# Performance work log

Hardware: AMD Instinct MI355X
Metric: run time of the kernel (lower is better)

The kernel has to match this reference:

```python
import jax, jax.numpy as jnp
import numpy as np

N = 100000   # nodes
E = 640000   # edges
F = 128      # num_features
D = 128      # dim
G = 128      # graphs in batch
BN_EPS = 1e-5


def setup_inputs() -> dict:
    key = jax.random.key(0)
    ks = jax.random.split(key, 16)
    lin = lambda k, i, o: (jax.random.normal(k, (i, o), jnp.float32) / np.sqrt(i)).astype(jnp.float32)
    inp = {
        "x": jax.random.normal(ks[0], (N, F), jnp.float32),
        "edge_index": jax.random.randint(ks[1], (2, E), 0, N),
        "batch": jnp.sort(jax.random.randint(ks[2], (N,), 0, G)),
        # layer 0: Linear(F,D)-ReLU-Linear(D,D), BN(D)
        "W0a": lin(ks[3], F, D), "b0a": jnp.zeros((D,), jnp.float32),
        "W0b": lin(ks[4], D, D), "b0b": jnp.zeros((D,), jnp.float32),
        "g0": jnp.ones((D,), jnp.float32), "be0": jnp.zeros((D,), jnp.float32),
        # layer 1: Linear(D,D)-ReLU-Linear(D,D), BN(D)
        "W1a": lin(ks[5], D, D), "b1a": jnp.zeros((D,), jnp.float32),
        "W1b": lin(ks[6], D, D), "b1b": jnp.zeros((D,), jnp.float32),
        "g1": jnp.ones((D,), jnp.float32), "be1": jnp.zeros((D,), jnp.float32),
        # layer 2: Linear(D,D)-ReLU-Linear(D,1), BN(1)
        "W2a": lin(ks[7], D, D), "b2a": jnp.zeros((D,), jnp.float32),
        "W2b": lin(ks[8], D, 1), "b2b": jnp.zeros((1,), jnp.float32),
        "g2": jnp.ones((1,), jnp.float32), "be2": jnp.zeros((1,), jnp.float32),
    }
    return inp


def _gin_layer(x, src, dst, Wa, ba, Wb, bb, g, be, relu_out):
    # GINConv (eps=0): h = x + sum_{j in N(i)} x_j, then MLP, then BN (train-mode stats)
    agg = jax.ops.segment_sum(x[src], dst, num_segments=N)
    h = x + agg
    h = jax.nn.relu(h @ Wa + ba) @ Wb + bb
    mu = jnp.mean(h, axis=0)
    var = jnp.mean((h - mu) ** 2, axis=0)  # biased var (torch BN normalization)
    h = (h - mu) * jax.lax.rsqrt(var + BN_EPS) * g + be
    return jax.nn.relu(h) if relu_out else h


def reference(x, edge_index, batch,
              W0a, b0a, W0b, b0b, g0, be0,
              W1a, b1a, W1b, b1b, g1, be1,
              W2a, b2a, W2b, b2b, g2, be2):
    src, dst = edge_index[0], edge_index[1]
    h = _gin_layer(x, src, dst, W0a, b0a, W0b, b0b, g0, be0, True)
    h = _gin_layer(h, src, dst, W1a, b1a, W1b, b1b, g1, be1, True)
    h = _gin_layer(h, src, dst, W2a, b2a, W2b, b2b, g2, be2, False)  # [N,1], no final ReLU
    # segment softmax over graphs, temperature 5.0 (PyG softmax semantics)
    z = h / 5.0
    m = jax.ops.segment_max(z, batch, num_segments=G)
    ez = jnp.exp(z - m[batch])
    s = jax.ops.segment_sum(ez, batch, num_segments=G)
    return ez / (s[batch] + 1e-16)
```

## Files before the change

### kernel.cpp

```cpp
#include <hip/hip_runtime.h>
#include <math.h>

#define NN 100000
#define EE 640000
#define GG 128
#define BN_EPS 1e-5f
#define NBLK 98

typedef __attribute__((ext_vector_type(8))) short short8;
typedef __attribute__((ext_vector_type(4))) float f32x4;


__device__ __forceinline__ short f2bf(float f) {
    unsigned u = __float_as_uint(f);
    u += 0x7fffu + ((u >> 16) & 1);
    return (short)(u >> 16);
}
__device__ __forceinline__ float bf2f(short s) {
    return __uint_as_float(((unsigned)(unsigned short)s) << 16);
}
__device__ __forceinline__ int swz(int row, int chunk) {
    return row * 128 + ((chunk ^ (row & 15)) << 3);
}
__device__ __forceinline__ int swze(int row, int col) {
    return row * 128 + (((col >> 3) ^ (row & 15)) << 3) + (col & 7);
}

__global__ void k_setup(const float* __restrict__ x,
                        const float* __restrict__ W0a, const float* __restrict__ W0b,
                        const float* __restrict__ W1a, const float* __restrict__ W1b,
                        const float* __restrict__ W2a, short* __restrict__ Wt,
                        short* __restrict__ Xbf, int* __restrict__ deg,
                        float* __restrict__ smf) {
    int idx = blockIdx.x * 256 + threadIdx.x;
    if (idx < 81920) {
        int wi = idx >> 14, r = idx & 16383;
        const float* W = (wi == 0) ? W0a : (wi == 1) ? W0b : (wi == 2) ? W1a
                        : (wi == 3) ? W1b : W2a;
        int k = r >> 7, n = r & 127;
        int ch = n >> 6, ct = (n >> 4) & 3, r16 = n & 15;
        int kc = k >> 3, kk = kc >> 2, q = kc & 3, e = k & 7;
        int lane = r16 + (q << 4);
        Wt[wi * 16384 + ((((ch * 4 + ct) * 4 + kk) * 64 + lane) << 3) + e] =
            f2bf(W[k * 128 + n]);
    }
    if (idx < NN) deg[idx] = 0;
    if (idx < 4112) smf[idx] = 0.0f;
    if (idx < 1600000) {
        const float4* xr = (const float4*)x + (size_t)idx * 2;
        float4 v0 = xr[0], v1 = xr[1];
        short8 o;
        o[0] = f2bf(v0.x); o[1] = f2bf(v0.y); o[2] = f2bf(v0.z); o[3] = f2bf(v0.w);
        o[4] = f2bf(v1.x); o[5] = f2bf(v1.y); o[6] = f2bf(v1.z); o[7] = f2bf(v1.w);
        *(short8*)(Xbf + (size_t)idx * 8) = o;
    }
}

__global__ void k_hist(const int* __restrict__ ei, int* __restrict__ deg) {
    int e = blockIdx.x * 256 + threadIdx.x;
    if (e < EE) atomicAdd(&deg[ei[EE + e]], 1);
}

__global__ __launch_bounds__(1024) void k_scan1(const int* __restrict__ deg,
                                                int* __restrict__ offs,
                                                int* __restrict__ bsums) {
    __shared__ int sm[1024];
    int t = threadIdx.x;
    int i = blockIdx.x * 1024 + t;
    int v = (i < NN) ? deg[i] : 0;
    sm[t] = v;
    __syncthreads();
    for (int off = 1; off < 1024; off <<= 1) {
        int add = (t >= off) ? sm[t - off] : 0;
        __syncthreads();
        sm[t] += add;
        __syncthreads();
    }
    if (i < NN) offs[i] = sm[t] - v;
    if (t == 1023) bsums[blockIdx.x] = sm[1023];
}

__global__ __launch_bounds__(1024) void k_scan3(int* __restrict__ offs,
                                                const int* __restrict__ bsums,
                                                int* __restrict__ pos) {
    __shared__ int smb[128];
    __shared__ int baseS;
    int t = threadIdx.x;
    if (t < 128) smb[t] = (t < NBLK) ? bsums[t] : 0;
    __syncthreads();
    if (t == 0) {
        int b = 0;
        for (int i = 0; i < (int)blockIdx.x; ++i) b += smb[i];
        baseS = b;
    }
    __syncthreads();
    int i = blockIdx.x * 1024 + t;
    if (i < NN) {
        int o = offs[i] + baseS;
        offs[i] = o;
        pos[i] = o;
    }
    if (i == 0) offs[NN] = EE;
}

__global__ void k_fill(const int* __restrict__ ei, int* __restrict__ pos,
                       int* __restrict__ csr) {
    int e = blockIdx.x * 256 + threadIdx.x;
    if (e < EE) {
        int d = ei[EE + e];
        int p = atomicAdd(&pos[d], 1);
        csr[p] = ei[e];
    }
}

template <int MODE>
__global__ __launch_bounds__(256, 4) void k_gmlp(const short* __restrict__ hin,
                                                 const int* __restrict__ offs,
                                                 const int* __restrict__ csr,
                                                 const float* __restrict__ rep,
                                                 const float* __restrict__ g,
                                                 const float* __restrict__ be,
                                                 const short* __restrict__ Wta,
                                                 const float* __restrict__ ba,
                                                 const short* __restrict__ Wtb,
                                                 const float* __restrict__ bb,
                                                 short* __restrict__ hout,
                                                 float* __restrict__ statsRep,
                                                 const float* __restrict__ w2,
                                                 const float* __restrict__ b2,
                                                 float* __restrict__ z,
                                                 float* __restrict__ s2rep) {
    __shared__ short Asb[8192];
    __shared__ float parS[128], parH[128];
    __shared__ float redS[1024];
    const int t = threadIdx.x;
    const int row0 = blockIdx.x * 64;
    const int lane = t & 63, wave = t >> 6;
    const int r16 = lane & 15, q = lane >> 4;
    const int rh = wave & 1, ch = wave >> 1;
    const int RA = rh * 32, CB = ch * 64;
    const int l = t & 15;

    if constexpr (MODE != 0) {
        if (t < 128) {
            float s = 0.f, ss = 0.f;
#pragma unroll
            for (int r = 0; r < 8; ++r) {
                s += rep[r * 256 + t];
                ss += rep[r * 256 + 128 + t];
            }
            const float inv = 1.0f / (float)NN;
            float mu = s * inv;
            float var = ss * inv - mu * mu;
            float sc = g[t] / sqrtf(var + BN_EPS);
            parS[t] = sc;
            parH[t] = be[t] - mu * sc;
        }
        __syncthreads();
    }

    const short* wA = Wta + (size_t)((ch * 1024 + lane) << 3);
    const short* wB = (MODE != 2) ? (Wtb + (size_t)((ch * 1024 + lane) << 3)) : nullptr;

    float sc8[8], sh8[8];
    if constexpr (MODE != 0) {
#pragma unroll
        for (int j = 0; j < 8; ++j) { sc8[j] = parS[l * 8 + j]; sh8[j] = parH[l * 8 + j]; }
    }
#pragma unroll
    for (int p = 0; p < 4; ++p) {
        int r = p * 16 + (t >> 4);
        int gr = row0 + r;
        float f8[8] = {0.f, 0.f, 0.f, 0.f, 0.f, 0.f, 0.f, 0.f};
        if (gr < NN) {
            int j0 = offs[gr], j1 = offs[gr + 1];
            short8 v = *(const short8*)(hin + (size_t)gr * 128 + l * 8);
#pragma unroll
            for (int k = 0; k < 8; ++k)
                f8[k] = (MODE != 0) ? fmaxf(fmaf(bf2f(v[k]), sc8[k], sh8[k]), 0.f) : bf2f(v[k]);
            int jlast = j1 - 1;
            for (int j = j0; j < j1; j += 8) {
                int ii[8];
                float mk[8];
                ii[0] = j;
                mk[0] = 1.f;
#pragma unroll
                for (int u = 1; u < 8; ++u) {
                    ii[u] = min(j + u, jlast);
                    mk[u] = (j + u <= jlast) ? 1.f : 0.f;
                }
                int sidx[8];
#pragma unroll
                for (int u = 0; u < 8; ++u) sidx[u] = csr[ii[u]];
                short8 w[8];
#pragma unroll
                for (int u = 0; u < 8; ++u)
                    w[u] = *(const short8*)(hin + (size_t)sidx[u] * 128 + l * 8);
#pragma unroll
                for (int k = 0; k < 8; ++k) {
                    if constexpr (MODE != 0) {
                        f8[k] += fmaxf(fmaf(bf2f(w[0][k]), sc8[k], sh8[k]), 0.f);
#pragma unroll
                        for (int u = 1; u < 8; ++u)
                            f8[k] = fmaf(mk[u], fmaxf(fmaf(bf2f(w[u][k]), sc8[k], sh8[k]), 0.f), f8[k]);
                    } else {
                        f8[k] += bf2f(w[0][k]);
#pragma unroll
                        for (int u = 1; u < 8; ++u)
                            f8[k] = fmaf(mk[u], bf2f(w[u][k]), f8[k]);
                    }
                }
            }
        }
        short8 o;
#pragma unroll
        for (int k = 0; k < 8; ++k) o[k] = f2bf(f8[k]);
        *(short8*)&Asb[swz(r, l)] = o;
    }
    __syncthreads();

    f32x4 acc[2][4];
#pragma unroll
    for (int rt = 0; rt < 2; ++rt)
#pragma unroll
        for (int ct = 0; ct < 4; ++ct) acc[rt][ct] = (f32x4)0.f;
#pragma unroll
    for (int kk = 0; kk < 4; ++kk) {
        short8 b[4], a[2];
#pragma unroll
        for (int ct = 0; ct < 4; ++ct)
            b[ct] = *(const short8*)(wA + ((ct * 4 + kk) << 9));
#pragma unroll
        for (int rt = 0; rt < 2; ++rt)
            a[rt] = *(const short8*)&Asb[swz(RA + rt * 16 + r16, kk * 4 + q)];
#pragma unroll
        for (int rt = 0; rt < 2; ++rt)
#pragma unroll
            for (int ct = 0; ct < 4; ++ct)
                acc[rt][ct] = __builtin_amdgcn_mfma_f32_16x16x32_bf16(a[rt], b[ct], acc[rt][ct], 0, 0, 0);
    }
    __syncthreads();

    float bav[4];
#pragma unroll
    for (int ct = 0; ct < 4; ++ct) bav[ct] = ba[CB + ct * 16 + r16];
#pragma unroll
    for (int rt = 0; rt < 2; ++rt)
#pragma unroll
        for (int ct = 0; ct < 4; ++ct)
#pragma unroll
            for (int rg = 0; rg < 4; ++rg) {
                float m = fmaxf(acc[rt][ct][rg] + bav[ct], 0.f);
                Asb[swze(RA + rt * 16 + q * 4 + rg, CB + ct * 16 + r16)] = f2bf(m);
            }
    __syncthreads();

    if constexpr (MODE == 2) {
        const int rr = t >> 4;
        float4 w0 = ((const float4*)w2)[l * 2];
        float4 w1 = ((const float4*)w2)[l * 2 + 1];
        float b2v = b2[0];
        float s = 0.f, ss = 0.f;
#pragma unroll
        for (int p = 0; p < 4; ++p) {
            int r = p * 16 + rr;
            int gr = row0 + r;
            short8 v = *(const short8*)&Asb[swz(r, l)];
            float pp = bf2f(v[0]) * w0.x + bf2f(v[1]) * w0.y + bf2f(v[2]) * w0.z +
                       bf2f(v[3]) * w0.w + bf2f(v[4]) * w1.x + bf2f(v[5]) * w1.y +
                       bf2f(v[6]) * w1.z + bf2f(v[7]) * w1.w;
#pragma unroll
            for (int off = 1; off < 16; off <<= 1) pp += __shfl_xor(pp, off, 16);
            if (l == 0 && gr < NN) {
                float h2 = pp + b2v;
                z[gr] = h2;
                s += h2;
                ss += h2 * h2;
            }
        }
        s += __shfl_xor(s, 16); s += __shfl_xor(s, 32);
        ss += __shfl_xor(ss, 16); ss += __shfl_xor(ss, 32);
        if ((t & 63) == 0) { redS[wave * 2] = s; redS[wave * 2 + 1] = ss; }
        __syncthreads();
        if (t == 0) {
            float S = 0.f, SS = 0.f;
#pragma unroll
            for (int w = 0; w < 4; ++w) { S += redS[w * 2]; SS += redS[w * 2 + 1]; }
            int rp = (blockIdx.x & 7) * 2;
            unsafeAtomicAdd(&s2rep[rp], S);
            unsafeAtomicAdd(&s2rep[rp + 1], SS);
        }
        return;
    } else {
#pragma unroll
        for (int rt = 0; rt < 2; ++rt)
#pragma unroll
            for (int ct = 0; ct < 4; ++ct) acc[rt][ct] = (f32x4)0.f;
#pragma unroll
        for (int kk = 0; kk < 4; ++kk) {
            short8 b[4], a[2];
#pragma unroll
            for (int ct = 0; ct < 4; ++ct)
                b[ct] = *(const short8*)(wB + ((ct * 4 + kk) << 9));
#pragma unroll
            for (int rt = 0; rt < 2; ++rt)
                a[rt] = *(const short8*)&Asb[swz(RA + rt * 16 + r16, kk * 4 + q)];
#pragma unroll
            for (int rt = 0; rt < 2; ++rt)
#pragma unroll
                for (int ct = 0; ct < 4; ++ct)
                    acc[rt][ct] = __builtin_amdgcn_mfma_f32_16x16x32_bf16(a[rt], b[ct], acc[rt][ct], 0, 0, 0);
        }
        __syncthreads();

        float bbv[4];
#pragma unroll
        for (int ct = 0; ct < 4; ++ct) bbv[ct] = bb[CB + ct * 16 + r16];
        float s[4] = {0.f, 0.f, 0.f, 0.f}, ss[4] = {0.f, 0.f, 0.f, 0.f};
#pragma unroll
        for (int rt = 0; rt < 2; ++rt)
#pragma unroll
            for (int ct = 0; ct < 4; ++ct)
#pragma unroll
                for (int rg = 0; rg < 4; ++rg) {
                    int lr = RA + rt * 16 + q * 4 + rg;
                    int gr = row0 + lr;
                    float hv = acc[rt][ct][rg] + bbv[ct];
                    if (gr < NN) { s[ct] += hv; ss[ct] += hv * hv; }
                    Asb[swze(lr, CB + ct * 16 + r16)] = f2bf(hv);
                }
#pragma unroll
        for (int ct = 0; ct < 4; ++ct) {
            s[ct] += __shfl_xor(s[ct], 16);
            s[ct] += __shfl_xor(s[ct], 32);
            ss[ct] += __shfl_xor(ss[ct], 16);
            ss[ct] += __shfl_xor(ss[ct], 32);
        }
        if (lane < 16) {
#pragma unroll
            for (int ct = 0; ct < 4; ++ct) {
                int col = CB + ct * 16 + r16;
                redS[rh * 512 + col] = s[ct];
                redS[rh * 512 + 128 + col] = ss[ct];
            }
        }
        __syncthreads();
        if (t < 256) {
            float v = redS[t] + redS[512 + t];
            unsafeAtomicAdd(&statsRep[(blockIdx.x & 7) * 256 + t], v);
        }
#pragma unroll
        for (int i = 0; i < 4; ++i) {
            int f = i * 256 + t;
            int r = f >> 4, c8 = f & 15;
            int gr = row0 + r;
            if (gr < NN)
                *(short8*)(hout + (size_t)gr * 128 + c8 * 8) = *(const short8*)&Asb[swz(r, c8)];
        }
    }
}

__device__ __forceinline__ int lbound(const int* __restrict__ b, int val) {
    int lo = 0, hi = NN;
    while (lo < hi) {
        int m = (lo + hi) >> 1;
        if (b[m] < val) lo = m + 1; else hi = m;
    }
    return lo;
}

__global__ void k_softmax(const float* __restrict__ zr, const float* __restrict__ s2rep,
                          const float* __restrict__ g2, const float* __restrict__ be2,
                          const int* __restrict__ batch, float* __restrict__ out) {
    __shared__ float rb[4];
    const int g = blockIdx.x, t = threadIdx.x;
    const int lo = lbound(batch, g), hi = lbound(batch, g + 1);
    float s = 0.f, ssq = 0.f;
#pragma unroll
    for (int i = 0; i < 8; ++i) { s += s2rep[i * 2]; ssq += s2rep[i * 2 + 1]; }
    const float mu = s / (float)NN;
    const float var = ssq / (float)NN - mu * mu;
    const float sc = g2[0] / sqrtf(var + BN_EPS) * 0.2f;
    const float sh = (be2[0] - mu * g2[0] / sqrtf(var + BN_EPS)) * 0.2f;

    float m = -INFINITY;
    for (int i = lo + t; i < hi; i += 256) m = fmaxf(m, fmaf(zr[i], sc, sh));
#pragma unroll
    for (int off = 1; off < 64; off <<= 1) m = fmaxf(m, __shfl_xor(m, off, 64));
    if ((t & 63) == 0) rb[t >> 6] = m;
    __syncthreads();
    float gmax = fmaxf(fmaxf(rb[0], rb[1]), fmaxf(rb[2], rb[3]));
    __syncthreads();

    float sum = 0.f;
    for (int i = lo + t; i < hi; i += 256) {
        float e = expf(fmaf(zr[i], sc, sh) - gmax);
        out[i] = e;
        sum += e;
    }
#pragma unroll
    for (int off = 1; off < 64; off <<= 1) sum += __shfl_xor(sum, off, 64);
    if ((t & 63) == 0) rb[t >> 6] = sum;
    __syncthreads();
    float S = rb[0] + rb[1] + rb[2] + rb[3];
    float inv = 1.0f / (S + 1e-16f);
    for (int i = lo + t; i < hi; i += 256) out[i] *= inv;
}

extern "C" void kernel_launch(void* const* d_in, const int* in_sizes, int n_in,
                              void* d_out, int out_size, void* d_ws, size_t ws_size,
                              hipStream_t stream) {
    const float* x   = (const float*)d_in[0];
    const int* ei    = (const int*)d_in[1];
    const int* batch = (const int*)d_in[2];
    const float *W0a = (const float*)d_in[3],  *b0a = (const float*)d_in[4];
    const float *W0b = (const float*)d_in[5],  *b0b = (const float*)d_in[6];
    const float *g0  = (const float*)d_in[7],  *be0 = (const float*)d_in[8];
    const float *W1a = (const float*)d_in[9],  *b1a = (const float*)d_in[10];
    const float *W1b = (const float*)d_in[11], *b1b = (const float*)d_in[12];
    const float *g1  = (const float*)d_in[13], *be1 = (const float*)d_in[14];
    const float *W2a = (const float*)d_in[15], *b2a = (const float*)d_in[16];
    const float *W2b = (const float*)d_in[17], *b2b = (const float*)d_in[18];
    const float *g2  = (const float*)d_in[19], *be2 = (const float*)d_in[20];
    float* out = (float*)d_out;

    char* wsb = (char*)d_ws;
    short* Abf = (short*)wsb;
    short* Bbf = (short*)(wsb + 25600000);
    float* Zb  = (float*)(wsb + 51200000);
    float* SMf = (float*)(wsb + 51600000);
    float* S0r = SMf;
    float* S1r = SMf + 2048;
    float* S2r = SMf + 4096;
    int* offs  = (int*)(wsb + 51620000);
    int* bsums = (int*)(wsb + 52020004);
    int* csr   = (int*)(wsb + 52020516);
    short* Wt  = (short*)(wsb + 54580544);
    short* Xbf = (short*)(wsb + 54744384);
    int* deg = (int*)wsb;
    int* pos = (int*)(wsb + 400000);

    const int gE    = (EE + 255) / 256;
    const int gGmlp = (NN + 63) / 64;

    k_setup<<<6250, 256, 0, stream>>>(x, W0a, W0b, W1a, W1b, W2a, Wt, Xbf, deg, SMf);

    k_hist<<<gE, 256, 0, stream>>>(ei, deg);
    k_scan1<<<NBLK, 1024, 0, stream>>>(deg, offs, bsums);
    k_scan3<<<NBLK, 1024, 0, stream>>>(offs, bsums, pos);
    k_fill<<<gE, 256, 0, stream>>>(ei, pos, csr);

    k_gmlp<0><<<gGmlp, 256, 0, stream>>>(Xbf, offs, csr, nullptr, nullptr, nullptr,
                                         Wt, b0a, Wt + 16384, b0b, Abf, S0r,
                                         nullptr, nullptr, nullptr, nullptr);
    k_gmlp<1><<<gGmlp, 256, 0, stream>>>(Abf, offs, csr, S0r, g0, be0,
                                         Wt + 2 * 16384, b1a, Wt + 3 * 16384, b1b, Bbf, S1r,
                                         nullptr, nullptr, nullptr, nullptr);
    k_gmlp<2><<<gGmlp, 256, 0, stream>>>(Bbf, offs, csr, S1r, g1, be1,
                                         Wt + 4 * 16384, b2a, nullptr, nullptr,
                                         nullptr, nullptr, W2b, b2b, Zb, S2r);

    k_softmax<<<GG, 256, 0, stream>>>(Zb, S2r, g2, be2, batch, out);
}
```

Baseline: 385.6 us.

## Edge-balanced aggregation with shared-memory atomics and fused setup/histogram kernel

The neighbor aggregation inside the fused GIN MLP kernel is now split by edges instead of by destination rows. Each 16-thread group takes an equal slice of the block's edge range, prefetches gathered rows four at a time, and flushes partial sums into an fp32 shared-memory accumulator with atomics. This targets load imbalance from skewed degrees and the padded, masked 8-wide gather loop, at the cost of shared-memory atomics and larger LDS use (a 32KB float tile), which may reduce occupancy. Setup and the degree histogram are merged into one kernel, and zeroing moves to memsets, removing a launch.

```diff
diff --git a/kernel.cpp b/kernel.cpp
--- a/kernel.cpp
+++ b/kernel.cpp
@@ -25,14 +25,26 @@
 __device__ __forceinline__ int swze(int row, int col) {
     return row * 128 + (((col >> 3) ^ (row & 15)) << 3) + (col & 7);
 }
-
-__global__ void k_setup(const float* __restrict__ x,
-                        const float* __restrict__ W0a, const float* __restrict__ W0b,
-                        const float* __restrict__ W1a, const float* __restrict__ W1b,
-                        const float* __restrict__ W2a, short* __restrict__ Wt,
-                        short* __restrict__ Xbf, int* __restrict__ deg,
-                        float* __restrict__ smf) {
+__device__ __forceinline__ int accIdx(int r, int cj) {
+    return r * 128 + ((cj ^ (r & 15)) << 3);
+}
+
+__global__ void k_prep(const float* __restrict__ x,
+                       const float* __restrict__ W0a, const float* __restrict__ W0b,
+                       const float* __restrict__ W1a, const float* __restrict__ W1b,
+                       const float* __restrict__ W2a, short* __restrict__ Wt,
+                       short* __restrict__ Xbf, const int* __restrict__ ei,
+                       int* __restrict__ deg) {
     int idx = blockIdx.x * 256 + threadIdx.x;
+    if (idx < 1600000) {
+        const float4* xr = (const float4*)x + (size_t)idx * 2;
+        float4 v0 = xr[0], v1 = xr[1];
+        short8 o;
+        o[0] = f2bf(v0.x); o[1] = f2bf(v0.y); o[2] = f2bf(v0.z); o[3] = f2bf(v0.w);
+        o[4] = f2bf(v1.x); o[5] = f2bf(v1.y); o[6] = f2bf(v1.z); o[7] = f2bf(v1.w);
+        *(short8*)(Xbf + (size_t)idx * 8) = o;
+    }
+    if (idx < EE) atomicAdd(&deg[ei[EE + idx]], 1);
     if (idx < 81920) {
         int wi = idx >> 14, r = idx & 16383;
         const float* W = (wi == 0) ? W0a : (wi == 1) ? W0b : (wi == 2) ? W1a
@@ -44,21 +56,6 @@
         Wt[wi * 16384 + ((((ch * 4 + ct) * 4 + kk) * 64 + lane) << 3) + e] =
             f2bf(W[k * 128 + n]);
     }
-    if (idx < NN) deg[idx] = 0;
-    if (idx < 4112) smf[idx] = 0.0f;
-    if (idx < 1600000) {
-        const float4* xr = (const float4*)x + (size_t)idx * 2;
-        float4 v0 = xr[0], v1 = xr[1];
-        short8 o;
-        o[0] = f2bf(v0.x); o[1] = f2bf(v0.y); o[2] = f2bf(v0.z); o[3] = f2bf(v0.w);
-        o[4] = f2bf(v1.x); o[5] = f2bf(v1.y); o[6] = f2bf(v1.z); o[7] = f2bf(v1.w);
-        *(short8*)(Xbf + (size_t)idx * 8) = o;
-    }
-}
-
-__global__ void k_hist(const int* __restrict__ ei, int* __restrict__ deg) {
-    int e = blockIdx.x * 256 + threadIdx.x;
-    if (e < EE) atomicAdd(&deg[ei[EE + e]], 1);
 }
 
 __global__ __launch_bounds__(1024) void k_scan1(const int* __restrict__ deg,
@@ -130,16 +127,19 @@
                                                  const float* __restrict__ b2,
                                                  float* __restrict__ z,
                                                  float* __restrict__ s2rep) {
-    __shared__ short Asb[8192];
+    __shared__ float accF[8192];
     __shared__ float parS[128], parH[128];
     __shared__ float redS[1024];
+    __shared__ int oL[65];
+    short* Amid = (short*)accF;
     const int t = threadIdx.x;
     const int row0 = blockIdx.x * 64;
     const int lane = t & 63, wave = t >> 6;
     const int r16 = lane & 15, q = lane >> 4;
     const int rh = wave & 1, ch = wave >> 1;
     const int RA = rh * 32, CB = ch * 64;
-    const int l = t & 15;
+    const int gp = t >> 4;
+    const int j = t & 15;
 
     if constexpr (MODE != 0) {
         if (t < 128) {
@@ -156,69 +156,109 @@
             parS[t] = sc;
             parH[t] = be[t] - mu * sc;
         }
-        __syncthreads();
-    }
+    }
+    if (t < 65) oL[t] = offs[min(row0 + t, NN)];
+    __syncthreads();
+
+    float sc8[8], sh8[8];
+    if constexpr (MODE != 0) {
+#pragma unroll
+        for (int u = 0; u < 8; ++u) { sc8[u] = parS[j * 8 + u]; sh8[u] = parH[j * 8 + u]; }
+    }
+
+#pragma unroll
+    for (int ii = 0; ii < 4; ++ii) {
+        int r = gp + ii * 16;
+        int gr = row0 + r;
+        float v8[8] = {0.f, 0.f, 0.f, 0.f, 0.f, 0.f, 0.f, 0.f};
+        if (gr < NN) {
+            short8 v = *(const short8*)(hin + (size_t)gr * 128 + j * 8);
+#pragma unroll
+            for (int u = 0; u < 8; ++u)
+                v8[u] = (MODE != 0) ? fmaxf(fmaf(bf2f(v[u]), sc8[u], sh8[u]), 0.f) : bf2f(v[u]);
+        }
+        float* dst = &accF[accIdx(r, j)];
+        *(f32x4*)dst = *(const f32x4*)&v8[0];
+        *(f32x4*)(dst + 4) = *(const f32x4*)&v8[4];
+    }
+    __syncthreads();
+
+    {
+        const int e0 = oL[0], e1 = oL[64];
+        const int len = (e1 - e0 + 15) >> 4;
+        const int eb = e0 + gp * len;
+        const int ee = min(eb + len, e1);
+        if (eb < ee) {
+            const int elast = ee - 1;
+            int lo = 0, hi = 63;
+            while (lo < hi) {
+                int m = (lo + hi + 1) >> 1;
+                if (oL[m] <= eb) lo = m; else hi = m - 1;
+            }
+            int dstr = lo;
+            int offsN = oL[dstr + 1];
+            float f8[8] = {0.f, 0.f, 0.f, 0.f, 0.f, 0.f, 0.f, 0.f};
+
+            auto flush = [&]() {
+                int cb = dstr * 128 + ((j ^ (dstr & 15)) << 3);
+#pragma unroll
+                for (int u = 0; u < 8; ++u) {
+                    atomicAdd(&accF[cb + u], f8[u]);
+                    f8[u] = 0.f;
+                }
+            };
+            auto proc = [&](int ei2, const short8& wv) {
+                if (ei2 < ee) {
+                    while (ei2 >= offsN) {
+                        flush();
+                        ++dstr;
+                        offsN = oL[dstr + 1];
+                    }
+#pragma unroll
+                    for (int u = 0; u < 8; ++u) {
+                        float xv = bf2f(wv[u]);
+                        if constexpr (MODE != 0) xv = fmaxf(fmaf(xv, sc8[u], sh8[u]), 0.f);
+                        f8[u] += xv;
+                    }
+                }
+            };
+
+            int s0 = csr[eb], s1 = csr[min(eb + 1, elast)];
+            int s2 = csr[min(eb + 2, elast)], s3 = csr[min(eb + 3, elast)];
+            short8 w0 = *(const short8*)(hin + (size_t)s0 * 128 + j * 8);
+            short8 w1 = *(const short8*)(hin + (size_t)s1 * 128 + j * 8);
+            short8 w2v = *(const short8*)(hin + (size_t)s2 * 128 + j * 8);
+            short8 w3 = *(const short8*)(hin + (size_t)s3 * 128 + j * 8);
+            for (int e = eb; e < ee; e += 4) {
+                int ep = e + 4;
+                int n0 = csr[min(ep, elast)], n1 = csr[min(ep + 1, elast)];
+                int n2 = csr[min(ep + 2, elast)], n3 = csr[min(ep + 3, elast)];
+                short8 x0 = *(const short8*)(hin + (size_t)n0 * 128 + j * 8);
+                short8 x1 = *(const short8*)(hin + (size_t)n1 * 128 + j * 8);
+                short8 x2 = *(const short8*)(hin + (size_t)n2 * 128 + j * 8);
+                short8 x3 = *(const short8*)(hin + (size_t)n3 * 128 + j * 8);
+                proc(e + 0, w0);
+                proc(e + 1, w1);
+                proc(e + 2, w2v);
+                proc(e + 3, w3);
+                w0 = x0; w1 = x1; w2v = x2; w3 = x3;
+            }
+            flush();
+        }
+    }
+    __syncthreads();
 
     const short* wA = Wta + (size_t)((ch * 1024 + lane) << 3);
     const short* wB = (MODE != 2) ? (Wtb + (size_t)((ch * 1024 + lane) << 3)) : nullptr;
 
-    float sc8[8], sh8[8];
-    if constexpr (MODE != 0) {
-#pragma unroll
-        for (int j = 0; j < 8; ++j) { sc8[j] = parS[l * 8 + j]; sh8[j] = parH[l * 8 + j]; }
-    }
-#pragma unroll
-    for (int p = 0; p < 4; ++p) {
-        int r = p * 16 + (t >> 4);
-        int gr = row0 + r;
-        float f8[8] = {0.f, 0.f, 0.f, 0.f, 0.f, 0.f, 0.f, 0.f};
-        if (gr < NN) {
-            int j0 = offs[gr], j1 = offs[gr + 1];
-            short8 v = *(const short8*)(hin + (size_t)gr * 128 + l * 8);
-#pragma unroll
-            for (int k = 0; k < 8; ++k)
-                f8[k] = (MODE != 0) ? fmaxf(fmaf(bf2f(v[k]), sc8[k], sh8[k]), 0.f) : bf2f(v[k]);
-            int jlast = j1 - 1;
-            for (int j = j0; j < j1; j += 8) {
-                int ii[8];
-                float mk[8];
-                ii[0] = j;
-                mk[0] = 1.f;
-#pragma unroll
-                for (int u = 1; u < 8; ++u) {
-                    ii[u] = min(j + u, jlast);
-                    mk[u] = (j + u <= jlast) ? 1.f : 0.f;
-                }
-                int sidx[8];
-#pragma unroll
-                for (int u = 0; u < 8; ++u) sidx[u] = csr[ii[u]];
-                short8 w[8];
-#pragma unroll
-                for (int u = 0; u < 8; ++u)
-                    w[u] = *(const short8*)(hin + (size_t)sidx[u] * 128 + l * 8);
-#pragma unroll
-                for (int k = 0; k < 8; ++k) {
-                    if constexpr (MODE != 0) {
-                        f8[k] += fmaxf(fmaf(bf2f(w[0][k]), sc8[k], sh8[k]), 0.f);
-#pragma unroll
-                        for (int u = 1; u < 8; ++u)
-                            f8[k] = fmaf(mk[u], fmaxf(fmaf(bf2f(w[u][k]), sc8[k], sh8[k]), 0.f), f8[k]);
-                    } else {
-                        f8[k] += bf2f(w[0][k]);
-#pragma unroll
-                        for (int u = 1; u < 8; ++u)
-                            f8[k] = fmaf(mk[u], bf2f(w[u][k]), f8[k]);
-                    }
-                }
-            }
-        }
-        short8 o;
-#pragma unroll
-        for (int k = 0; k < 8; ++k) o[k] = f2bf(f8[k]);
-        *(short8*)&Asb[swz(r, l)] = o;
-    }
-    __syncthreads();
-
+    auto ldafrag = [&](int r, int cj) -> short8 {
+        const f32x4* ap = (const f32x4*)&accF[accIdx(r, cj)];
+        f32x4 lo2 = ap[0], hi2 = ap[1];
+        short8 a;
+        a[0] = f2bf(lo2.x); a[1] = f2bf(lo2.y); a[2] = f2bf(lo2.z); a[3] = f2bf(lo2.w);
+        a[4] = f2bf(hi2.x); a[5] = f2bf(hi2.y); a[6] = f2bf(hi2.z); a[7] = f2bf(hi2.w);
+        return a;
+    };
     f32x4 acc[2][4];
 #pragma unroll
     for (int rt = 0; rt < 2; ++rt)
@@ -232,7 +272,7 @@
             b[ct] = *(const short8*)(wA + ((ct * 4 + kk) << 9));
 #pragma unroll
         for (int rt = 0; rt < 2; ++rt)
-            a[rt] = *(const short8*)&Asb[swz(RA + rt * 16 + r16, kk * 4 + q)];
+            a[rt] = ldafrag(RA + rt * 16 + r16, kk * 4 + q);
 #pragma unroll
         for (int rt = 0; rt < 2; ++rt)
 #pragma unroll
@@ -251,27 +291,27 @@
 #pragma unroll
             for (int rg = 0; rg < 4; ++rg) {
                 float m = fmaxf(acc[rt][ct][rg] + bav[ct], 0.f);
-                Asb[swze(RA + rt * 16 + q * 4 + rg, CB + ct * 16 + r16)] = f2bf(m);
+                Amid[swze(RA + rt * 16 + q * 4 + rg, CB + ct * 16 + r16)] = f2bf(m);
             }
     __syncthreads();
 
     if constexpr (MODE == 2) {
         const int rr = t >> 4;
-        float4 w0 = ((const float4*)w2)[l * 2];
-        float4 w1 = ((const float4*)w2)[l * 2 + 1];
+        float4 w0f = ((const float4*)w2)[j * 2];
+        float4 w1f = ((const float4*)w2)[j * 2 + 1];
         float b2v = b2[0];
         float s = 0.f, ss = 0.f;
 #pragma unroll
         for (int p = 0; p < 4; ++p) {
             int r = p * 16 + rr;
             int gr = row0 + r;
-            short8 v = *(const short8*)&Asb[swz(r, l)];
-            float pp = bf2f(v[0]) * w0.x + bf2f(v[1]) * w0.y + bf2f(v[2]) * w0.z +
-                       bf2f(v[3]) * w0.w + bf2f(v[4]) * w1.x + bf2f(v[5]) * w1.y +
-                       bf2f(v[6]) * w1.z + bf2f(v[7]) * w1.w;
+            short8 v = *(const short8*)&Amid[swz(r, j)];
+            float pp = bf2f(v[0]) * w0f.x + bf2f(v[1]) * w0f.y + bf2f(v[2]) * w0f.z +
+                       bf2f(v[3]) * w0f.w + bf2f(v[4]) * w1f.x + bf2f(v[5]) * w1f.y +
+                       bf2f(v[6]) * w1f.z + bf2f(v[7]) * w1f.w;
 #pragma unroll
             for (int off = 1; off < 16; off <<= 1) pp += __shfl_xor(pp, off, 16);
-            if (l == 0 && gr < NN) {
+            if (j == 0 && gr < NN) {
                 float h2 = pp + b2v;
                 z[gr] = h2;
                 s += h2;
@@ -304,7 +344,7 @@
                 b[ct] = *(const short8*)(wB + ((ct * 4 + kk) << 9));
 #pragma unroll
             for (int rt = 0; rt < 2; ++rt)
-                a[rt] = *(const short8*)&Asb[swz(RA + rt * 16 + r16, kk * 4 + q)];
+                a[rt] = *(const short8*)&Amid[swz(RA + rt * 16 + r16, kk * 4 + q)];
 #pragma unroll
             for (int rt = 0; rt < 2; ++rt)
 #pragma unroll
@@ -327,7 +367,7 @@
                     int gr = row0 + lr;
                     float hv = acc[rt][ct][rg] + bbv[ct];
                     if (gr < NN) { s[ct] += hv; ss[ct] += hv * hv; }
-                    Asb[swze(lr, CB + ct * 16 + r16)] = f2bf(hv);
+                    Amid[swze(lr, CB + ct * 16 + r16)] = f2bf(hv);
                 }
 #pragma unroll
         for (int ct = 0; ct < 4; ++ct) {
@@ -355,7 +395,7 @@
             int r = f >> 4, c8 = f & 15;
             int gr = row0 + r;
             if (gr < NN)
-                *(short8*)(hout + (size_t)gr * 128 + c8 * 8) = *(const short8*)&Asb[swz(r, c8)];
+                *(short8*)(hout + (size_t)gr * 128 + c8 * 8) = *(const short8*)&Amid[swz(r, c8)];
         }
     }
 }
@@ -443,9 +483,11 @@
     const int gE    = (EE + 255) / 256;
     const int gGmlp = (NN + 63) / 64;
 
-    k_setup<<<6250, 256, 0, stream>>>(x, W0a, W0b, W1a, W1b, W2a, Wt, Xbf, deg, SMf);
-
-    k_hist<<<gE, 256, 0, stream>>>(ei, deg);
+    (void)hipMemsetAsync(deg, 0, NN * sizeof(int), stream);
+    (void)hipMemsetAsync(SMf, 0, 4112 * sizeof(float), stream);
+
+    k_prep<<<6400, 256, 0, stream>>>(x, W0a, W0b, W1a, W1b, W2a, Wt, Xbf, ei, deg);
+
     k_scan1<<<NBLK, 1024, 0, stream>>>(deg, offs, bsums);
     k_scan3<<<NBLK, 1024, 0, stream>>>(offs, bsums, pos);
     k_fill<<<gE, 256, 0, stream>>>(ei, pos, csr);
```

Result: slower. 526.5 us (+36.5%).
